# Performance work log

Measured on AMD Instinct MI355X. Metric: run time of the kernel, lower is better.

The kernel has to match this reference:

```python
import jax, jax.numpy as jnp
import numpy as np

B, S, H, E, V, EXTRA = 128, 512, 1024, 1024, 50000, 500
EPS = 1e-8


def setup_inputs() -> dict:
    key = jax.random.key(0)
    ks = jax.random.split(key, 32)
    sc = 0.02
    n = lambda k, sh: (jax.random.normal(k, sh, jnp.float32) * sc)
    return {
        'inputs': jax.random.randint(ks[0], (B, 1), 0, V),
        'dec_hidden': n(ks[1], (1, B, H)),
        'enc_outputs': n(ks[2], (B, S, H)),
        'enc_padding_mask': jnp.zeros((B, S), jnp.float32),
        'context_vector_t1': n(ks[3], (B, H)),
        'enc_batch_extend_vocab': jax.random.randint(ks[4], (B, S), 0, V + EXTRA),
        'extra_zeros': jnp.zeros((B, EXTRA), jnp.float32),
        'coverage': jax.random.uniform(ks[5], (B, S), jnp.float32) * 0.1,
        # parameters
        'embed': n(ks[6], (V, E)),
        'ln_g': jnp.ones((E,), jnp.float32),
        'ln_b': jnp.zeros((E,), jnp.float32),
        'xc_W': n(ks[7], (E, H + E)), 'xc_b': jnp.zeros((E,), jnp.float32),
        'W_ih': n(ks[8], (3 * H, E)), 'W_hh': n(ks[9], (3 * H, H)),
        'b_ih': jnp.zeros((3 * H,), jnp.float32), 'b_hh': jnp.zeros((3 * H,), jnp.float32),
        'Wh': n(ks[10], (H, H)),
        'Ws': n(ks[11], (H, H)), 'Ws_b': jnp.zeros((H,), jnp.float32),
        'Wc': n(ks[12], (H, 1)),
        'Vv': n(ks[13], (H,)),
        'pg_W': n(ks[14], (2 * H + E,)), 'pg_b': jnp.zeros((1,), jnp.float32),
        'out1_W': n(ks[15], (H, 2 * H)), 'out1_b': jnp.zeros((H,), jnp.float32),
        'out2_W': n(ks[16], (V, H)), 'out2_b': jnp.zeros((V,), jnp.float32),
    }


def _layernorm(x, g, b):
    mu = jnp.mean(x, axis=-1, keepdims=True)
    var = jnp.mean(jnp.square(x - mu), axis=-1, keepdims=True)
    return (x - mu) / jnp.sqrt(var + 1e-5) * g + b


def reference(inputs, dec_hidden, enc_outputs, enc_padding_mask, context_vector_t1,
              enc_batch_extend_vocab, extra_zeros, coverage,
              embed, ln_g, ln_b, xc_W, xc_b, W_ih, W_hh, b_ih, b_hh,
              Wh, Ws, Ws_b, Wc, Vv, pg_W, pg_b, out1_W, out1_b, out2_W, out2_b):
    # embedding + layernorm: [B, E]
    x = _layernorm(embed[inputs[:, 0]], ln_g, ln_b)
    # x_context: Linear(H+E -> E)
    x = jnp.concatenate([x, context_vector_t1], axis=1) @ xc_W.T + xc_b

    # single GRU step (torch gate order r, z, n)
    h0 = dec_hidden[0]  # [B, H]
    gx = x @ W_ih.T + b_ih
    gh = h0 @ W_hh.T + b_hh
    r = jax.nn.sigmoid(gx[:, :H] + gh[:, :H])
    z = jax.nn.sigmoid(gx[:, H:2 * H] + gh[:, H:2 * H])
    nn_ = jnp.tanh(gx[:, 2 * H:] + r * gh[:, 2 * H:])
    s_t = (1.0 - z) * nn_ + z * h0  # [B, H]; dec_output == s_t for 1-layer GRU
    dec_output = s_t

    # Bahdanau additive attention with coverage
    enc_feat = jnp.einsum('bsh,kh->bsk', enc_outputs, Wh)           # [B,S,H]
    dec_feat = s_t @ Ws.T + Ws_b                                     # [B,H]
    cov_feat = coverage[:, :, None] * Wc[:, 0][None, None, :]        # [B,S,H]
    e_t = jnp.einsum('bsh,h->bs', jnp.tanh(enc_feat + dec_feat[:, None, :] + cov_feat), Vv)
    atten_dist = jax.nn.softmax(e_t + enc_padding_mask, axis=1)      # [B,S]
    h_t = jnp.einsum('bs,bsh->bh', atten_dist, enc_outputs)          # [B,H]
    coverage_next = coverage + atten_dist

    # pointer generator gate
    p_gen_in = jnp.concatenate([h_t, s_t, x], axis=1)                # [B, 2H+E]
    p_gen = jnp.clip(jax.nn.sigmoid(p_gen_in @ pg_W + pg_b), EPS, None)[:, None]  # [B,1]

    # vocab distribution
    s_t_h_t = jnp.concatenate([dec_output, h_t], axis=1)             # [B,2H]
    logits = (s_t_h_t @ out1_W.T + out1_b) @ out2_W.T + out2_b       # [B,V]
    vocab_dist = jax.nn.softmax(logits, axis=1)

    # mix + scatter-add copy distribution over extended vocab
    vocab_dist_ = jnp.concatenate([p_gen * vocab_dist, extra_zeros], axis=1)  # [B, V+EXTRA]
    atten_dist_ = (1.0 - p_gen) * atten_dist
    rows = jnp.arange(B)[:, None]
    final_dist = vocab_dist_.at[rows, enc_batch_extend_vocab].add(atten_dist_)
    final_dist = jnp.clip(final_dist, EPS, None)

    coverage_loss = jnp.sum(jnp.minimum(atten_dist, coverage_next), axis=1)  # [B]
    return (jnp.log(final_dist), s_t[None], h_t, coverage_next, coverage_loss)
```

## Files before the change

kernel.cpp:

```cpp
#include <hip/hip_runtime.h>
#include <hip/hip_bf16.h>
#include <stdint.h>

#define B_ 128
#define S_ 512
#define H_ 1024
#define E_ 1024
#define V_ 50000
#define EXTRA_ 500
#define VE_ 50500
#define EPS_ 1e-8f

typedef __attribute__((ext_vector_type(4))) float f32x4;
typedef __attribute__((ext_vector_type(8))) short bf16x8;

__device__ __forceinline__ unsigned short f2bf(float f) {
    unsigned u = __builtin_bit_cast(unsigned, f);
    u = (u + 0x7FFFu + ((u >> 16) & 1u)) >> 16;
    return (unsigned short)u;
}

__device__ __forceinline__ bf16x8 pack8(const float* f) {
    union { bf16x8 v; unsigned short s[8]; } u;
#pragma unroll
    for (int i = 0; i < 8; ++i) u.s[i] = f2bf(f[i]);
    return u.v;
}

__device__ __forceinline__ float bf2f(unsigned short s) {
    unsigned u = (unsigned)s << 16;
    return __builtin_bit_cast(float, u);
}

__device__ __forceinline__ float fast_tanh(float x) {
    x = fminf(fmaxf(x, -15.f), 15.f);
    float e = __expf(2.f * x);
    return __fdividef(e - 1.f, e + 1.f);
}

__device__ __forceinline__ void gload16(const void* g, void* l) {
    __builtin_amdgcn_global_load_lds(
        reinterpret_cast<const __attribute__((address_space(1))) unsigned int*>(
            reinterpret_cast<uintptr_t>(g)),
        reinterpret_cast<__attribute__((address_space(3))) unsigned int*>(
            reinterpret_cast<uintptr_t>(l)),
        16, 0, 0);
}

__global__ __launch_bounds__(256) void cvt_bf16_kernel(const float* __restrict__ in,
                                                       unsigned short* __restrict__ out) {
    int i = (blockIdx.x * 256 + threadIdx.x) * 8;
    float f[8];
    *(float4*)f     = *(const float4*)(in + i);
    *(float4*)(f+4) = *(const float4*)(in + i + 4);
    union { uint4 v; unsigned short s[8]; } u;
#pragma unroll
    for (int j = 0; j < 8; ++j) u.s[j] = f2bf(f[j]);
    *(uint4*)(out + i) = u.v;
}

__global__ __launch_bounds__(256) void embed_ln_kernel(
    const int* __restrict__ tok, const float* __restrict__ embed,
    const float* __restrict__ g, const float* __restrict__ beta,
    const float* __restrict__ ctx, float* __restrict__ x_cat)
{
    __shared__ float red[256];
    int b = blockIdx.x, t = threadIdx.x;
    const float* row = embed + (size_t)tok[b] * E_;
    float v[4];
    float s = 0.f;
#pragma unroll
    for (int i = 0; i < 4; ++i) { v[i] = row[t + i*256]; s += v[i]; }
    red[t] = s; __syncthreads();
    for (int o = 128; o > 0; o >>= 1) { if (t < o) red[t] += red[t+o]; __syncthreads(); }
    float mu = red[0] * (1.f/E_);
    __syncthreads();
    s = 0.f;
#pragma unroll
    for (int i = 0; i < 4; ++i) { float d = v[i]-mu; s += d*d; }
    red[t] = s; __syncthreads();
    for (int o = 128; o > 0; o >>= 1) { if (t < o) red[t] += red[t+o]; __syncthreads(); }
    float inv = rsqrtf(red[0]*(1.f/E_) + 1e-5f);
    float* xrow = x_cat + (size_t)b * 2048;
#pragma unroll
    for (int i = 0; i < 4; ++i) {
        int j = t + i*256;
        xrow[j] = (v[i]-mu)*inv*g[j] + beta[j];
        xrow[1024 + j] = ctx[b*1024 + j];
    }
}

__global__ __launch_bounds__(256) void gemm128_kernel(
    const float* __restrict__ A, const float* __restrict__ W,
    const float* __restrict__ bias, float* __restrict__ C,
    int N, int K, int ldc, int kchunk)
{
    __shared__ char Ab[128*64*2];
    __shared__ char Wb[64*64*2];
    const int t = threadIdx.x;
    const int wid = t >> 6, lane = t & 63;
    const int waveM = wid >> 1, waveN = wid & 1;
    const int lq = lane >> 4, lr = lane & 15;
    const int n0 = blockIdx.x * 64;
    const int kbeg = blockIdx.y * kchunk, kend = kbeg + kchunk;
    f32x4 acc[4][2];
#pragma unroll
    for (int i = 0; i < 4; ++i)
#pragma unroll
        for (int j = 0; j < 2; ++j) acc[i][j] = (f32x4){0.f,0.f,0.f,0.f};
    for (int kc = kbeg; kc < kend; kc += 64) {
        __syncthreads();
#pragma unroll
        for (int i = 0; i < 4; ++i) {
            int c = t + i*256;
            int row = c >> 3, k8 = (c & 7) << 3;
            const float* src = A + (size_t)row*K + kc + k8;
            float f[8];
            *(float4*)f     = *(const float4*)src;
            *(float4*)(f+4) = *(const float4*)(src+4);
            int byte = row*128 + ((k8*2) ^ ((row&7)<<4));
            *(bf16x8*)(Ab + byte) = pack8(f);
        }
#pragma unroll
        for (int i = 0; i < 2; ++i) {
            int c = t + i*256;
            int row = c >> 3, k8 = (c & 7) << 3;
            int n = n0 + row;
            float f[8] = {0,0,0,0,0,0,0,0};
            if (n < N) {
                const float* src = W + (size_t)n*K + kc + k8;
                *(float4*)f     = *(const float4*)src;
                *(float4*)(f+4) = *(const float4*)(src+4);
            }
            int byte = row*128 + ((k8*2) ^ ((row&7)<<4));
            *(bf16x8*)(Wb + byte) = pack8(f);
        }
        __syncthreads();
#pragma unroll
        for (int kf = 0; kf < 2; ++kf) {
            int kk2 = (kf*32 + (lq<<3)) * 2;
            bf16x8 bfr[2];
#pragma unroll
            for (int nf = 0; nf < 2; ++nf) {
                int r = waveN*32 + nf*16 + lr;
                bfr[nf] = *(const bf16x8*)(Wb + r*128 + (kk2 ^ ((r&7)<<4)));
            }
#pragma unroll
            for (int mf = 0; mf < 4; ++mf) {
                int r = waveM*64 + mf*16 + lr;
                bf16x8 afr = *(const bf16x8*)(Ab + r*128 + (kk2 ^ ((r&7)<<4)));
#pragma unroll
                for (int nf = 0; nf < 2; ++nf)
                    acc[mf][nf] = __builtin_amdgcn_mfma_f32_16x16x32_bf16(afr, bfr[nf], acc[mf][nf], 0, 0, 0);
            }
        }
    }
    float* Cp = C + (size_t)blockIdx.y * 128 * (size_t)ldc;
    bool addb = (bias != nullptr) && (blockIdx.y == 0);
#pragma unroll
    for (int mf = 0; mf < 4; ++mf)
#pragma unroll
        for (int nf = 0; nf < 2; ++nf) {
            int n = n0 + waveN*32 + nf*16 + lr;
            if (n < N) {
                float bv = addb ? bias[n] : 0.f;
#pragma unroll
                for (int r = 0; r < 4; ++r) {
                    int m = waveM*64 + mf*16 + (lq<<2) + r;
                    Cp[(size_t)m*ldc + n] = acc[mf][nf][r] + bv;
                }
            }
        }
}

__global__ __launch_bounds__(256) void reduce4_kernel(
    const float* __restrict__ in, float* __restrict__ out, int len)
{
    int i = blockIdx.x*256 + threadIdx.x;
    if (i < len) out[i] = in[i] + in[len+i] + in[2*len+i] + in[3*len+i];
}

__global__ __launch_bounds__(256) void gru_gate_kernel(
    const float* __restrict__ gxp, const float* __restrict__ ghp,
    const float* __restrict__ h0, float* __restrict__ s_t)
{
    int i = blockIdx.x*256 + threadIdx.x;
    int b = i >> 10, h = i & 1023;
    const float* gx0 = gxp + (size_t)b*3072;
    const float* gx1 = gx0 + 393216;
    const float* gh0 = ghp + (size_t)b*3072;
    const float* gh1 = gh0 + 393216;
    float grx = gx0[h] + gx1[h],        grh = gh0[h] + gh1[h];
    float gzx = gx0[h+1024]+gx1[h+1024], gzh = gh0[h+1024]+gh1[h+1024];
    float gnx = gx0[h+2048]+gx1[h+2048], gnh = gh0[h+2048]+gh1[h+2048];
    float r = 1.f/(1.f+__expf(-(grx + grh)));
    float z = 1.f/(1.f+__expf(-(gzx + gzh)));
    float n = fast_tanh(gnx + r*gnh);
    s_t[i] = (1.f-z)*n + z*h0[i];
}

__global__ __launch_bounds__(256,4) void attn_gemm_bf16_kernel(
    const unsigned short* __restrict__ encb,
    const unsigned short* __restrict__ whb,
    const float* __restrict__ dec_feat, const float* __restrict__ coverage,
    const float* __restrict__ Wc, const float* __restrict__ Vv,
    float* __restrict__ e_part)
{
    __shared__ char Ab[128*128];
    __shared__ char Bb[128*128];
    const int t = threadIdx.x;
    const int wid = t >> 6, lane = t & 63;
    const int waveM = wid >> 1, waveN = wid & 1;
    const int lq = lane >> 4, lr = lane & 15;
    int bid = blockIdx.x;
    int wg = (bid & 7) * 512 + (bid >> 3);
    const int nt = wg & 7, mt = wg >> 3;
    const int m0 = mt * 128, n0 = nt * 128;
    const int b = m0 >> 9;

    const int grow = wid*8 + (lane >> 3);
    const int gk16 = (lane & 7) ^ ((lane >> 3) & 7);
    const unsigned short* asrc = encb + (size_t)(m0 + grow)*H_ + gk16*8;
    const unsigned short* bsrc = whb  + (size_t)(n0 + grow)*H_ + gk16*8;
    char* aldst = Ab + wid*1024;
    char* bldst = Bb + wid*1024;

    f32x4 acc[4][4];
#pragma unroll
    for (int i = 0; i < 4; ++i)
#pragma unroll
        for (int j = 0; j < 4; ++j) acc[i][j] = (f32x4){0.f,0.f,0.f,0.f};

    for (int kc = 0; kc < 1024; kc += 64) {
        __syncthreads();
#pragma unroll
        for (int i = 0; i < 4; ++i) {
            gload16(asrc + kc + i*32*H_, aldst + i*4096);
            gload16(bsrc + kc + i*32*H_, bldst + i*4096);
        }
        __syncthreads();
#pragma unroll
        for (int kf = 0; kf < 2; ++kf) {
            const int koff = kf*64 + lq*16;
            bf16x8 bfr[4];
#pragma unroll
            for (int nf = 0; nf < 4; ++nf) {
                int r = waveN*64 + nf*16 + lr;
                bfr[nf] = *(const bf16x8*)(Bb + r*128 + (koff ^ ((r&7)<<4)));
            }
#pragma unroll
            for (int mf = 0; mf < 4; ++mf) {
                int r = waveM*64 + mf*16 + lr;
                bf16x8 afr = *(const bf16x8*)(Ab + r*128 + (koff ^ ((r&7)<<4)));
#pragma unroll
                for (int nf = 0; nf < 4; ++nf)
                    acc[mf][nf] = __builtin_amdgcn_mfma_f32_16x16x32_bf16(afr, bfr[nf], acc[mf][nf], 0, 0, 0);
            }
        }
    }
    float cv[4][4];
#pragma unroll
    for (int mf = 0; mf < 4; ++mf)
#pragma unroll
        for (int r = 0; r < 4; ++r) {
            int m = m0 + waveM*64 + mf*16 + lq*4 + r;
            cv[mf][r] = coverage[b*S_ + (m & 511)];
        }
    float e_acc[4][4] = {};
#pragma unroll
    for (int nf = 0; nf < 4; ++nf) {
        int n = n0 + waveN*64 + nf*16 + lr;
        float df = dec_feat[b*H_ + n];
        float wc = Wc[n];
        float vv = Vv[n];
#pragma unroll
        for (int mf = 0; mf < 4; ++mf)
#pragma unroll
            for (int r = 0; r < 4; ++r)
                e_acc[mf][r] += fast_tanh(acc[mf][nf][r] + df + cv[mf][r]*wc) * vv;
    }
#pragma unroll
    for (int msk = 1; msk < 16; msk <<= 1)
#pragma unroll
        for (int mf = 0; mf < 4; ++mf)
#pragma unroll
            for (int r = 0; r < 4; ++r)
                e_acc[mf][r] += __shfl_xor(e_acc[mf][r], msk);
    __syncthreads();
    float* el = (float*)Ab;
    if (lr == 0) {
#pragma unroll
        for (int mf = 0; mf < 4; ++mf)
#pragma unroll
            for (int r = 0; r < 4; ++r)
                el[waveN*128 + waveM*64 + mf*16 + lq*4 + r] = e_acc[mf][r];
    }
    __syncthreads();
    if (t < 128)
        e_part[(size_t)nt*65536 + m0 + t] = el[t] + el[128 + t];
}

__global__ __launch_bounds__(512,4) void attn_gemm_f32_kernel(
    const float* __restrict__ enc, const float* __restrict__ Wh,
    const float* __restrict__ dec_feat, const float* __restrict__ coverage,
    const float* __restrict__ Wc, const float* __restrict__ Vv,
    float* __restrict__ e_part)
{
    __shared__ char Ab[128*64*2];
    __shared__ char Bb[256*64*2];
    __shared__ float e_lds[4][128];
    const int t = threadIdx.x;
    const int wid = t >> 6, lane = t & 63;
    const int waveM = wid >> 2, waveN = wid & 3;
    const int lq = lane >> 4, lr = lane & 15;
    int bid = blockIdx.x;
    int wg = (bid & 7) * 256 + (bid >> 3);
    const int mt = wg >> 2, nt = wg & 3;
    const int m0 = mt * 128, n0 = nt * 256;
    const int b = m0 >> 9;
    const int arow = t >> 2, ak0 = (t & 3) * 16;
    const int brow = t >> 1, bk0 = (t & 1) * 32;
    f32x4 acc[4][4];
#pragma unroll
    for (int i = 0; i < 4; ++i)
#pragma unroll
        for (int j = 0; j < 4; ++j) acc[i][j] = (f32x4){0.f,0.f,0.f,0.f};
    for (int kc = 0; kc < 1024; kc += 64) {
        __syncthreads();
        {
            const float* src = enc + (size_t)(m0 + arow)*H_ + kc + ak0;
            float f[16];
            *(float4*)(f)    = *(const float4*)(src);
            *(float4*)(f+4)  = *(const float4*)(src+4);
            *(float4*)(f+8)  = *(const float4*)(src+8);
            *(float4*)(f+12) = *(const float4*)(src+12);
            char* dst = Ab + arow*128;
            int sw = (arow & 7) << 4;
            *(bf16x8*)(dst + ((ak0*2)      ^ sw)) = pack8(f);
            *(bf16x8*)(dst + ((ak0*2 + 16) ^ sw)) = pack8(f+8);
        }
        {
            const float* src = Wh + (size_t)(n0 + brow)*H_ + kc + bk0;
            char* dst = Bb + brow*128;
            int sw = (brow & 7) << 4;
            float f[16];
            *(float4*)(f)    = *(const float4*)(src);
            *(float4*)(f+4)  = *(const float4*)(src+4);
            *(float4*)(f+8)  = *(const float4*)(src+8);
            *(float4*)(f+12) = *(const float4*)(src+12);
            *(bf16x8*)(dst + ((bk0*2)      ^ sw)) = pack8(f);
            *(bf16x8*)(dst + ((bk0*2 + 16) ^ sw)) = pack8(f+8);
            *(float4*)(f)    = *(const float4*)(src+16);
            *(float4*)(f+4)  = *(const float4*)(src+20);
            *(float4*)(f+8)  = *(const float4*)(src+24);
            *(float4*)(f+12) = *(const float4*)(src+28);
            *(bf16x8*)(dst + ((bk0*2 + 32) ^ sw)) = pack8(f);
            *(bf16x8*)(dst + ((bk0*2 + 48) ^ sw)) = pack8(f+8);
        }
        __syncthreads();
#pragma unroll
        for (int kf = 0; kf < 2; ++kf) {
            const int koff = kf*64 + lq*16;
            bf16x8 bfr[4];
#pragma unroll
            for (int nf = 0; nf < 4; ++nf) {
                int r = waveN*64 + nf*16 + lr;
                bfr[nf] = *(const bf16x8*)(Bb + r*128 + (koff ^ ((r&7)<<4)));
            }
#pragma unroll
            for (int mf = 0; mf < 4; ++mf) {
                int r = waveM*64 + mf*16 + lr;
                bf16x8 afr = *(const bf16x8*)(Ab + r*128 + (koff ^ ((r&7)<<4)));
#pragma unroll
                for (int nf = 0; nf < 4; ++nf)
                    acc[mf][nf] = __builtin_amdgcn_mfma_f32_16x16x32_bf16(afr, bfr[nf], acc[mf][nf], 0, 0, 0);
            }
        }
    }
    float cv[4][4];
#pragma unroll
    for (int mf = 0; mf < 4; ++mf)
#pragma unroll
        for (int r = 0; r < 4; ++r) {
            int m = m0 + waveM*64 + mf*16 + lq*4 + r;
            cv[mf][r] = coverage[b*S_ + (m & 511)];
        }
    float e_acc[4][4] = {};
#pragma unroll
    for (int nf = 0; nf < 4; ++nf) {
        int n = n0 + waveN*64 + nf*16 + lr;
        float df = dec_feat[b*H_ + n];
        float wc = Wc[n];
        float vv = Vv[n];
#pragma unroll
        for (int mf = 0; mf < 4; ++mf)
#pragma unroll
            for (int r = 0; r < 4; ++r)
                e_acc[mf][r] += fast_tanh(acc[mf][nf][r] + df + cv[mf][r]*wc) * vv;
    }
#pragma unroll
    for (int msk = 1; msk < 16; msk <<= 1)
#pragma unroll
        for (int mf = 0; mf < 4; ++mf)
#pragma unroll
            for (int r = 0; r < 4; ++r)
                e_acc[mf][r] += __shfl_xor(e_acc[mf][r], msk);
    if (lr == 0) {
#pragma unroll
        for (int mf = 0; mf < 4; ++mf)
#pragma unroll
            for (int r = 0; r < 4; ++r)
                e_lds[waveN][waveM*64 + mf*16 + lq*4 + r] = e_acc[mf][r];
    }
    __syncthreads();
    if (t < 128)
        e_part[(size_t)nt*65536 + m0 + t] = e_lds[0][t] + e_lds[1][t] + e_lds[2][t] + e_lds[3][t];
}

__global__ __launch_bounds__(256) void attn_softmax_kernel(
    const float* __restrict__ e_part, int np, const float* __restrict__ mask,
    const float* __restrict__ cov, float* __restrict__ att,
    float* __restrict__ cov_next, float* __restrict__ loss)
{
    __shared__ float red[256];
    int b = blockIdx.x, t = threadIdx.x;
    int i1 = b*S_ + t, i2 = i1 + 256;
    float e1 = mask[i1], e2 = mask[i2];
    for (int p = 0; p < np; ++p) { e1 += e_part[(size_t)p*65536 + i1]; e2 += e_part[(size_t)p*65536 + i2]; }
    red[t] = fmaxf(e1, e2); __syncthreads();
    for (int o = 128; o > 0; o >>= 1) { if (t < o) red[t] = fmaxf(red[t], red[t+o]); __syncthreads(); }
    float m = red[0]; __syncthreads();
    float a1 = __expf(e1-m), a2 = __expf(e2-m);
    red[t] = a1+a2; __syncthreads();
    for (int o = 128; o > 0; o >>= 1) { if (t < o) red[t] += red[t+o]; __syncthreads(); }
    float inv = 1.f/red[0]; __syncthreads();
    a1 *= inv; a2 *= inv;
    att[i1] = a1; att[i2] = a2;
    float c1 = cov[i1]+a1, c2 = cov[i2]+a2;
    cov_next[i1] = c1; cov_next[i2] = c2;
    red[t] = fminf(a1,c1)+fminf(a2,c2); __syncthreads();
    for (int o = 128; o > 0; o >>= 1) { if (t < o) red[t] += red[t+o]; __syncthreads(); }
    if (t == 0) loss[b] = red[0];
}

__global__ __launch_bounds__(256) void context_part_bf16_kernel(
    const float* __restrict__ att, const unsigned short* __restrict__ encb, float* __restrict__ hq)
{
    __shared__ float asl[128];
    int b = blockIdx.x, sub = blockIdx.y;
    int hh = sub & 1, q = sub >> 1;
    int t = threadIdx.x;
    if (t < 128) asl[t] = att[b*S_ + q*128 + t];
    __syncthreads();
    int h = hh*512 + t*2;
    const unsigned short* ep = encb + (size_t)b*S_*H_ + (size_t)q*128*H_ + h;
    float a0 = 0.f, a1 = 0.f;
#pragma unroll 4
    for (int s = 0; s < 128; ++s) {
        union { unsigned u; unsigned short s2[2]; } v;
        v.u = *(const unsigned*)(ep + (size_t)s*H_);
        float w = asl[s];
        a0 += w*bf2f(v.s2[0]); a1 += w*bf2f(v.s2[1]);
    }
    float* o = hq + ((size_t)q*B_ + b)*H_ + h;
    o[0] = a0; o[1] = a1;
}

__global__ __launch_bounds__(256) void context_part_f32_kernel(
    const float* __restrict__ att, const float* __restrict__ enc, float* __restrict__ hq)
{
    __shared__ float asl[128];
    int b = blockIdx.x, sub = blockIdx.y;
    int hh = sub & 1, q = sub >> 1;
    int t = threadIdx.x;
    if (t < 128) asl[t] = att[b*S_ + q*128 + t];
    __syncthreads();
    int h = hh*512 + t*2;
    const float* ep = enc + (size_t)b*S_*H_ + (size_t)q*128*H_ + h;
    float a0 = 0.f, a1 = 0.f;
#pragma unroll 4
    for (int s = 0; s < 128; ++s) {
        float2 v = *(const float2*)(ep + (size_t)s*H_);
        float w = asl[s];
        a0 += w*v.x; a1 += w*v.y;
    }
    float* o = hq + ((size_t)q*B_ + b)*H_ + h;
    o[0] = a0; o[1] = a1;
}

__global__ __launch_bounds__(256) void pgen_kernel(
    const float* __restrict__ h_t, const float* __restrict__ s_t, const float* __restrict__ x,
    const float* __restrict__ pgW, const float* __restrict__ pgb,
    float* __restrict__ pgen, float* __restrict__ A2)
{
    __shared__ float red[256];
    int b = blockIdx.x, t = threadIdx.x;
    float s = 0.f;
#pragma unroll
    for (int i = 0; i < 12; ++i) {
        int j = t + i*256;
        float v = (j < 1024) ? h_t[b*1024+j] : (j < 2048 ? s_t[b*1024 + j-1024] : x[b*1024 + j-2048]);
        s += v * pgW[j];
    }
    red[t] = s; __syncthreads();
    for (int o = 128; o > 0; o >>= 1) { if (t < o) red[t] += red[t+o]; __syncthreads(); }
    if (t == 0) {
        float p = 1.f/(1.f+__expf(-(red[0] + pgb[0])));
        pgen[b] = fmaxf(p, EPS_);
    }
#pragma unroll
    for (int i = 0; i < 8; ++i) {
        int j = t + i*256;
        A2[(size_t)b*2048 + j] = (j < 1024) ? s_t[b*1024+j] : h_t[b*1024+j-1024];
    }
}

__global__ __launch_bounds__(1024) void vocab_softmax_kernel(
    float* __restrict__ out0, const float* __restrict__ pgen)
{
    __shared__ float rm[1024], rl[1024];
    int b = blockIdx.x, t = threadIdx.x;
    float* row = out0 + (size_t)b*VE_;
    float m = -1e30f, l = 0.f;
    for (int i = t; i < V_; i += 1024) {
        float xv = row[i];
        if (xv > m) { l = l*__expf(m-xv) + 1.f; m = xv; }
        else l += __expf(xv-m);
    }
    rm[t] = m; rl[t] = l; __syncthreads();
    for (int o = 512; o > 0; o >>= 1) {
        if (t < o) {
            float m1 = rm[t], m2 = rm[t+o];
            float M = fmaxf(m1, m2);
            rl[t] = rl[t]*__expf(m1-M) + rl[t+o]*__expf(m2-M);
            rm[t] = M;
        }
        __syncthreads();
    }
    float M = rm[0], inv = pgen[b]/rl[0];
    for (int i = t; i < V_; i += 1024)
        row[i] = __expf(row[i]-M)*inv;
    for (int i = V_ + t; i < VE_; i += 1024)
        row[i] = 0.f;
}

__global__ __launch_bounds__(256) void scatter_kernel(
    const int* __restrict__ ebev, const float* __restrict__ att,
    const float* __restrict__ pgen, float* __restrict__ out0)
{
    int i = blockIdx.x*256 + threadIdx.x;
    int b = i >> 9;
    float val = (1.f - pgen[b]) * att[i];
    int col = ebev[i];
    atomicAdd(out0 + (size_t)b*VE_ + col, val);
}

__global__ __launch_bounds__(256) void log_kernel(float* __restrict__ out0)
{
    int i = (blockIdx.x*256 + threadIdx.x) * 4;
    if (i >= B_*VE_) return;
    float4 v = *(float4*)(out0 + i);
    v.x = __logf(fmaxf(v.x, EPS_));
    v.y = __logf(fmaxf(v.y, EPS_));
    v.z = __logf(fmaxf(v.z, EPS_));
    v.w = __logf(fmaxf(v.w, EPS_));
    *(float4*)(out0 + i) = v;
}

extern "C" void kernel_launch(void* const* d_in, const int* in_sizes, int n_in,
                              void* d_out, int out_size, void* d_ws, size_t ws_size,
                              hipStream_t stream) {
    const int*   tok        = (const int*)d_in[0];
    const float* dec_hidden = (const float*)d_in[1];
    const float* enc        = (const float*)d_in[2];
    const float* mask       = (const float*)d_in[3];
    const float* ctx1       = (const float*)d_in[4];
    const int*   ebev       = (const int*)d_in[5];
    const float* cov        = (const float*)d_in[7];
    const float* embed      = (const float*)d_in[8];
    const float* ln_g       = (const float*)d_in[9];
    const float* ln_b       = (const float*)d_in[10];
    const float* xc_W       = (const float*)d_in[11];
    const float* xc_b       = (const float*)d_in[12];
    const float* W_ih       = (const float*)d_in[13];
    const float* W_hh       = (const float*)d_in[14];
    const float* b_ih       = (const float*)d_in[15];
    const float* b_hh       = (const float*)d_in[16];
    const float* Wh         = (const float*)d_in[17];
    const float* Ws         = (const float*)d_in[18];
    const float* Ws_b       = (const float*)d_in[19];
    const float* Wc         = (const float*)d_in[20];
    const float* Vv         = (const float*)d_in[21];
    const float* pg_W       = (const float*)d_in[22];
    const float* pg_b       = (const float*)d_in[23];
    const float* out1_W     = (const float*)d_in[24];
    const float* out1_b     = (const float*)d_in[25];
    const float* out2_W     = (const float*)d_in[26];
    const float* out2_b     = (const float*)d_in[27];

    float* out      = (float*)d_out;
    float* s_t      = out + 6464000;
    float* h_t      = out + 6595072;
    float* cov_next = out + 6726144;
    float* loss     = out + 6791680;

    const size_t ENC_SLOTS = 33554432, WH_SLOTS = 524288;
    const size_t need = (ENC_SLOTS + WH_SLOTS + 5177472) * 4;
    const bool bf16_path = (ws_size >= need);

    float* wsf = (float*)d_ws;
    unsigned short* enc_bf = (unsigned short*)d_ws;
    unsigned short* wh_bf  = (unsigned short*)(wsf + ENC_SLOTS);
    float* base     = bf16_path ? (wsf + ENC_SLOTS + WH_SLOTS) : wsf;
    float* x_cat    = base;
    float* x_part   = base + 262144;
    float* x        = base + 786432;
    float* gx_part  = base + 917504;
    float* gh_part  = base + 1703936;
    float* ds_part  = base + 2490368;
    float* dec_feat = base + 3014656;
    float* e_part   = base + 3145728;
    float* att      = base + 3670016;
    float* pgen     = base + 3735552;
    float* A2       = base + 3735680;
    float* h2_part  = base + 3997824;
    float* h2       = base + 4522112;
    float* hq       = base + 4653184;

    if (bf16_path) {
        cvt_bf16_kernel<<<32768, 256, 0, stream>>>(enc, enc_bf);
        cvt_bf16_kernel<<<512, 256, 0, stream>>>(Wh, wh_bf);
    }
    embed_ln_kernel<<<128, 256, 0, stream>>>(tok, embed, ln_g, ln_b, ctx1, x_cat);
    gemm128_kernel<<<dim3(16,4), 256, 0, stream>>>(x_cat, xc_W, xc_b, x_part, 1024, 2048, 1024, 512);
    reduce4_kernel<<<512, 256, 0, stream>>>(x_part, x, 131072);
    gemm128_kernel<<<dim3(48,2), 256, 0, stream>>>(x, W_ih, b_ih, gx_part, 3072, 1024, 3072, 512);
    gemm128_kernel<<<dim3(48,2), 256, 0, stream>>>(dec_hidden, W_hh, b_hh, gh_part, 3072, 1024, 3072, 512);
    gru_gate_kernel<<<512, 256, 0, stream>>>(gx_part, gh_part, dec_hidden, s_t);
    gemm128_kernel<<<dim3(16,4), 256, 0, stream>>>(s_t, Ws, Ws_b, ds_part, 1024, 1024, 1024, 256);
    reduce4_kernel<<<512, 256, 0, stream>>>(ds_part, dec_feat, 131072);

    int npart;
    if (bf16_path) {
        attn_gemm_bf16_kernel<<<4096, 256, 0, stream>>>(enc_bf, wh_bf, dec_feat, cov, Wc, Vv, e_part);
        npart = 8;
    } else {
        attn_gemm_f32_kernel<<<2048, 512, 0, stream>>>(enc, Wh, dec_feat, cov, Wc, Vv, e_part);
        npart = 4;
    }
    attn_softmax_kernel<<<128, 256, 0, stream>>>(e_part, npart, mask, cov, att, cov_next, loss);
    dim3 g8(128, 8);
    if (bf16_path)
        context_part_bf16_kernel<<<g8, 256, 0, stream>>>(att, enc_bf, hq);
    else
        context_part_f32_kernel<<<g8, 256, 0, stream>>>(att, enc, hq);
    reduce4_kernel<<<512, 256, 0, stream>>>(hq, h_t, 131072);
    pgen_kernel<<<128, 256, 0, stream>>>(h_t, s_t, x, pg_W, pg_b, pgen, A2);
    gemm128_kernel<<<dim3(16,4), 256, 0, stream>>>(A2, out1_W, out1_b, h2_part, 1024, 2048, 1024, 512);
    reduce4_kernel<<<512, 256, 0, stream>>>(h2_part, h2, 131072);
    gemm128_kernel<<<dim3(782,1), 256, 0, stream>>>(h2, out2_W, out2_b, out, 50000, 1024, VE_, 1024);
    vocab_softmax_kernel<<<128, 1024, 0, stream>>>(out, pgen);
    scatter_kernel<<<256, 256, 0, stream>>>(ebev, att, pgen, out);
    log_kernel<<<6313, 256, 0, stream>>>(out);
}
```

Measured before the change: 528.2 us.

## Fuse vocab softmax, copy scatter and log; split-K the vocab projection

Merges the vocab softmax, the pointer scatter-add and the log pass into one kernel per row. The copy distribution goes into a shared-memory hash table and is looked up during the final write, which drops a full read-modify-write pass over the output and the global atomics. The vocab GEMM gets a two-way K split into a separate workspace buffer when enough workspace is available, and the fused kernel sums the two partials during both of its passes. The softmax loops now use float4 loads. The cost is a hash probe for every output element and extra partial-logit traffic in the split path.

```diff
diff --git a/kernel.cpp b/kernel.cpp
--- a/kernel.cpp
+++ b/kernel.cpp
@@ -92,7 +92,7 @@
 
 __global__ __launch_bounds__(256) void gemm128_kernel(
     const float* __restrict__ A, const float* __restrict__ W,
-    const float* __restrict__ bias, float* __restrict__ C,
+    const float* __restrict__ bias, float* __restrict__ C, float* __restrict__ C1,
     int N, int K, int ldc, int kchunk)
 {
     __shared__ char Ab[128*64*2];
@@ -155,7 +155,7 @@
             }
         }
     }
-    float* Cp = C + (size_t)blockIdx.y * 128 * (size_t)ldc;
+    float* Cp = (blockIdx.y == 0) ? C : (C1 + (size_t)(blockIdx.y - 1) * 128 * (size_t)ldc);
     bool addb = (bias != nullptr) && (blockIdx.y == 0);
 #pragma unroll
     for (int mf = 0; mf < 4; ++mf)
@@ -515,17 +515,50 @@
     }
 }
 
-__global__ __launch_bounds__(1024) void vocab_softmax_kernel(
-    float* __restrict__ out0, const float* __restrict__ pgen)
+__device__ __forceinline__ float hlookup(const unsigned* hkey, const float* hval, unsigned col) {
+    unsigned slot = (col * 2654435761u >> 16) & 1023u;
+    while (true) {
+        unsigned k = hkey[slot];
+        if (k == 0xFFFFFFFFu) return 0.f;
+        if (k == col) return hval[slot];
+        slot = (slot + 1) & 1023u;
+    }
+}
+
+__global__ __launch_bounds__(1024) void vocab_fused_kernel(
+    const float* __restrict__ p0, const float* __restrict__ p1, int two,
+    const float* __restrict__ pgen, const int* __restrict__ ebev,
+    const float* __restrict__ att, float* __restrict__ out0)
 {
     __shared__ float rm[1024], rl[1024];
+    __shared__ unsigned hkey[1024];
+    __shared__ float hval[1024];
     int b = blockIdx.x, t = threadIdx.x;
-    float* row = out0 + (size_t)b*VE_;
+    hkey[t] = 0xFFFFFFFFu; hval[t] = 0.f;
+    __syncthreads();
+    float pg = pgen[b];
+    if (t < 512) {
+        unsigned col = (unsigned)ebev[b*S_ + t];
+        float v = (1.f - pg) * att[b*S_ + t];
+        unsigned slot = (col * 2654435761u >> 16) & 1023u;
+        while (true) {
+            unsigned old = atomicCAS(&hkey[slot], 0xFFFFFFFFu, col);
+            if (old == 0xFFFFFFFFu || old == col) { atomicAdd(&hval[slot], v); break; }
+            slot = (slot + 1) & 1023u;
+        }
+    }
+    const float* r0 = p0 + (size_t)b*VE_;
+    const float* r1 = p1 ? (p1 + (size_t)b*VE_) : r0;
     float m = -1e30f, l = 0.f;
-    for (int i = t; i < V_; i += 1024) {
-        float xv = row[i];
-        if (xv > m) { l = l*__expf(m-xv) + 1.f; m = xv; }
-        else l += __expf(xv-m);
+    for (int i = t*4; i < V_; i += 4096) {
+        float4 v = *(const float4*)(r0 + i);
+        if (two) {
+            float4 w = *(const float4*)(r1 + i);
+            v.x += w.x; v.y += w.y; v.z += w.z; v.w += w.w;
+        }
+        float mx = fmaxf(fmaxf(v.x, v.y), fmaxf(v.z, v.w));
+        if (mx > m) { l *= __expf(m - mx); m = mx; }
+        l += __expf(v.x-m) + __expf(v.y-m) + __expf(v.z-m) + __expf(v.w-m);
     }
     rm[t] = m; rl[t] = l; __syncthreads();
     for (int o = 512; o > 0; o >>= 1) {
@@ -537,34 +570,23 @@
         }
         __syncthreads();
     }
-    float M = rm[0], inv = pgen[b]/rl[0];
-    for (int i = t; i < V_; i += 1024)
-        row[i] = __expf(row[i]-M)*inv;
+    float M = rm[0], inv = pg / rl[0];
+    float* orow = out0 + (size_t)b*VE_;
+    for (int i = t*4; i < V_; i += 4096) {
+        float4 v = *(const float4*)(r0 + i);
+        if (two) {
+            float4 w = *(const float4*)(r1 + i);
+            v.x += w.x; v.y += w.y; v.z += w.z; v.w += w.w;
+        }
+        float4 o;
+        o.x = __logf(fmaxf(__expf(v.x-M)*inv + hlookup(hkey, hval, i),   EPS_));
+        o.y = __logf(fmaxf(__expf(v.y-M)*inv + hlookup(hkey, hval, i+1), EPS_));
+        o.z = __logf(fmaxf(__expf(v.z-M)*inv + hlookup(hkey, hval, i+2), EPS_));
+        o.w = __logf(fmaxf(__expf(v.w-M)*inv + hlookup(hkey, hval, i+3), EPS_));
+        *(float4*)(orow + i) = o;
+    }
     for (int i = V_ + t; i < VE_; i += 1024)
-        row[i] = 0.f;
-}
-
-__global__ __launch_bounds__(256) void scatter_kernel(
-    const int* __restrict__ ebev, const float* __restrict__ att,
-    const float* __restrict__ pgen, float* __restrict__ out0)
-{
-    int i = blockIdx.x*256 + threadIdx.x;
-    int b = i >> 9;
-    float val = (1.f - pgen[b]) * att[i];
-    int col = ebev[i];
-    atomicAdd(out0 + (size_t)b*VE_ + col, val);
-}
-
-__global__ __launch_bounds__(256) void log_kernel(float* __restrict__ out0)
-{
-    int i = (blockIdx.x*256 + threadIdx.x) * 4;
-    if (i >= B_*VE_) return;
-    float4 v = *(float4*)(out0 + i);
-    v.x = __logf(fmaxf(v.x, EPS_));
-    v.y = __logf(fmaxf(v.y, EPS_));
-    v.z = __logf(fmaxf(v.z, EPS_));
-    v.w = __logf(fmaxf(v.w, EPS_));
-    *(float4*)(out0 + i) = v;
+        orow[i] = __logf(fmaxf(hlookup(hkey, hval, i), EPS_));
 }
 
 extern "C" void kernel_launch(void* const* d_in, const int* in_sizes, int n_in,
@@ -605,8 +627,12 @@
     float* loss     = out + 6791680;
 
     const size_t ENC_SLOTS = 33554432, WH_SLOTS = 524288;
-    const size_t need = (ENC_SLOTS + WH_SLOTS + 5177472) * 4;
+    const size_t BASE_SLOTS = 5177472;
+    const size_t P1_SLOTS = 6464000;
+    const size_t need  = (ENC_SLOTS + WH_SLOTS + BASE_SLOTS) * 4;
+    const size_t need2 = (ENC_SLOTS + WH_SLOTS + BASE_SLOTS + P1_SLOTS) * 4;
     const bool bf16_path = (ws_size >= need);
+    const bool split2 = bf16_path && (ws_size >= need2);
 
     float* wsf = (float*)d_ws;
     unsigned short* enc_bf = (unsigned short*)d_ws;
@@ -626,18 +652,19 @@
     float* h2_part  = base + 3997824;
     float* h2       = base + 4522112;
     float* hq       = base + 4653184;
+    float* logit_p1 = base + 5177472;
 
     if (bf16_path) {
         cvt_bf16_kernel<<<32768, 256, 0, stream>>>(enc, enc_bf);
         cvt_bf16_kernel<<<512, 256, 0, stream>>>(Wh, wh_bf);
     }
     embed_ln_kernel<<<128, 256, 0, stream>>>(tok, embed, ln_g, ln_b, ctx1, x_cat);
-    gemm128_kernel<<<dim3(16,4), 256, 0, stream>>>(x_cat, xc_W, xc_b, x_part, 1024, 2048, 1024, 512);
+    gemm128_kernel<<<dim3(16,4), 256, 0, stream>>>(x_cat, xc_W, xc_b, x_part, x_part + 131072, 1024, 2048, 1024, 512);
     reduce4_kernel<<<512, 256, 0, stream>>>(x_part, x, 131072);
-    gemm128_kernel<<<dim3(48,2), 256, 0, stream>>>(x, W_ih, b_ih, gx_part, 3072, 1024, 3072, 512);
-    gemm128_kernel<<<dim3(48,2), 256, 0, stream>>>(dec_hidden, W_hh, b_hh, gh_part, 3072, 1024, 3072, 512);
+    gemm128_kernel<<<dim3(48,2), 256, 0, stream>>>(x, W_ih, b_ih, gx_part, gx_part + 393216, 3072, 1024, 3072, 512);
+    gemm128_kernel<<<dim3(48,2), 256, 0, stream>>>(dec_hidden, W_hh, b_hh, gh_part, gh_part + 393216, 3072, 1024, 3072, 512);
     gru_gate_kernel<<<512, 256, 0, stream>>>(gx_part, gh_part, dec_hidden, s_t);
-    gemm128_kernel<<<dim3(16,4), 256, 0, stream>>>(s_t, Ws, Ws_b, ds_part, 1024, 1024, 1024, 256);
+    gemm128_kernel<<<dim3(16,4), 256, 0, stream>>>(s_t, Ws, Ws_b, ds_part, ds_part + 131072, 1024, 1024, 1024, 256);
     reduce4_kernel<<<512, 256, 0, stream>>>(ds_part, dec_feat, 131072);
 
     int npart;
@@ -656,10 +683,14 @@
         context_part_f32_kernel<<<g8, 256, 0, stream>>>(att, enc, hq);
     reduce4_kernel<<<512, 256, 0, stream>>>(hq, h_t, 131072);
     pgen_kernel<<<128, 256, 0, stream>>>(h_t, s_t, x, pg_W, pg_b, pgen, A2);
-    gemm128_kernel<<<dim3(16,4), 256, 0, stream>>>(A2, out1_W, out1_b, h2_part, 1024, 2048, 1024, 512);
+    gemm128_kernel<<<dim3(16,4), 256, 0, stream>>>(A2, out1_W, out1_b, h2_part, h2_part + 131072, 1024, 2048, 1024, 512);
     reduce4_kernel<<<512, 256, 0, stream>>>(h2_part, h2, 131072);
-    gemm128_kernel<<<dim3(782,1), 256, 0, stream>>>(h2, out2_W, out2_b, out, 50000, 1024, VE_, 1024);
-    vocab_softmax_kernel<<<128, 1024, 0, stream>>>(out, pgen);
-    scatter_kernel<<<256, 256, 0, stream>>>(ebev, att, pgen, out);
-    log_kernel<<<6313, 256, 0, stream>>>(out);
-}
+
+    if (split2) {
+        gemm128_kernel<<<dim3(782,2), 256, 0, stream>>>(h2, out2_W, out2_b, out, logit_p1, 50000, 1024, VE_, 512);
+        vocab_fused_kernel<<<128, 1024, 0, stream>>>(out, logit_p1, 1, pgen, ebev, att, out);
+    } else {
+        gemm128_kernel<<<dim3(782,1), 256, 0, stream>>>(h2, out2_W, out2_b, out, nullptr, 50000, 1024, VE_, 1024);
+        vocab_fused_kernel<<<128, 1024, 0, stream>>>(out, nullptr, 0, pgen, ebev, att, out);
+    }
+}
```

Result: slower. 685.3 us (+29.7%).
